# Kernel tuning notes

Measured on AMD Instinct MI355X. Metric: run time of the kernel, lower is better.

## Reference

```python
import jax, jax.numpy as jnp
import numpy as np

B, N, M, C = 4, 4096, 4096, 256
IMG_W, IMG_H = 1242.0, 376.0  # KITTI-like image extents for keypoint coords


def setup_inputs() -> dict:
    key = jax.random.key(0)
    ks = jax.random.split(key, 12)
    s = 1.0 / np.sqrt(C)
    scale_uv = jnp.array([IMG_W, IMG_H], dtype=jnp.float32)
    return {
        "nodes_L": jax.random.normal(ks[0], (B, N, C), jnp.float32),
        "nodes_R": jax.random.normal(ks[1], (B, M, C), jnp.float32),
        "kpts_L": jax.random.uniform(ks[2], (B, N, 2), jnp.float32) * scale_uv,
        "kpts_R": jax.random.uniform(ks[3], (B, M, 2), jnp.float32) * scale_uv,
        "Wq": jax.random.normal(ks[4], (C, C), jnp.float32) * s,
        "bq": jnp.zeros((C,), jnp.float32),
        "Wk": jax.random.normal(ks[5], (C, C), jnp.float32) * s,
        "bk": jnp.zeros((C,), jnp.float32),
        "Wv": jax.random.normal(ks[6], (C, C), jnp.float32) * s,
        "bv": jnp.zeros((C,), jnp.float32),
        "Wm": jax.random.normal(ks[7], (C, C), jnp.float32) * s,
        "bm": jnp.zeros((C,), jnp.float32),
    }


def reference(nodes_L, nodes_R, kpts_L, kpts_R, Wq, bq, Wk, bk, Wv, bv, Wm, bm):
    dim = nodes_L.shape[-1]
    # torch.nn.Linear: y = x @ W.T + b  (W is [out, in])
    Q = jnp.einsum('bnc,dc->bnd', nodes_L, Wq) + bq  # [B,N,C]
    K = jnp.einsum('bmc,dc->bmd', nodes_R, Wk) + bk  # [B,M,C]
    V = jnp.einsum('bmc,dc->bmd', nodes_R, Wv) + bv  # [B,M,C]

    # Epipolar geometric mask from keypoint coordinates
    dist_v = jnp.abs(kpts_L[:, :, 1:2] - kpts_R[:, None, :, 1])  # [B,N,M]
    dist_u = kpts_L[:, :, 0:1] - kpts_R[:, None, :, 0]           # [B,N,M]
    mask = (dist_v < 3.0) & (dist_u > 0) & (dist_u < 192)

    attn = jnp.einsum('bnd,bmd->bnm', Q, K) / (dim ** 0.5)       # [B,N,M]
    attn = jnp.where(mask, attn, jnp.float32(-1e9))
    attn_weights = jax.nn.softmax(attn, axis=-1)                 # [B,N,M]

    matched_features = jnp.einsum('bnm,bmd->bnd', attn_weights, V)
    init_disparity = jnp.sum(attn_weights * dist_u, axis=-1, keepdims=True)  # [B,N,1]
    confidence = jnp.any(mask, axis=-1, keepdims=True).astype(jnp.float32)   # [B,N,1]
    out = jnp.einsum('bnd,cd->bnc', matched_features, Wm) + bm   # [B,N,C]
    return (out, init_disparity, confidence, attn_weights)
```

## Files before the change

### kernel.cpp

```cpp
#include <hip/hip_runtime.h>
#include <stdint.h>

#define CAP 192

typedef __attribute__((ext_vector_type(4))) float f32x4;
typedef __attribute__((ext_vector_type(8))) short bf16x8;

__device__ __forceinline__ float bf2f(ushort u) {
  return __uint_as_float(((unsigned)u) << 16);
}
__device__ __forceinline__ ushort f2bf(float f) {
  unsigned u = __float_as_uint(f);
  return (ushort)((u + 0x7fffu + ((u >> 16) & 1u)) >> 16);
}
__device__ __forceinline__ float wredsum(float v) {
#pragma unroll
  for (int o = 32; o; o >>= 1) v += __shfl_xor(v, o);
  return v;
}

template <bool A_BF16, typename OutT>
__device__ __forceinline__ void gemm_body(const void* __restrict__ Av,
                                          const float* __restrict__ Wf,
                                          const float* __restrict__ bias,
                                          OutT* __restrict__ Y, int blk,
                                          ushort* As, ushort* Bs) {
  int tid = threadIdx.x;
  int lane = tid & 63, wid = tid >> 6;
  int bm = blk >> 1, bn = blk & 1;
  int r0 = bm * 128, c0 = bn * 128;
  int wr = wid >> 1, wc = wid & 1;
  f32x4 acc[4][4] = {};
  for (int k0 = 0; k0 < 256; k0 += 32) {
    __syncthreads();
#pragma unroll
    for (int p = 0; p < 2; ++p) {
      int u = p * 2048 + tid * 8;
      int row = u >> 5, col = u & 31;
      if constexpr (A_BF16) {
        *(bf16x8*)&As[u] =
            *(const bf16x8*)((const ushort*)Av + (size_t)(r0 + row) * 256 + k0 + col);
      } else {
        const float* Af = (const float*)Av;
        float4 lo = *(const float4*)(Af + (size_t)(r0 + row) * 256 + k0 + col);
        float4 hi = *(const float4*)(Af + (size_t)(r0 + row) * 256 + k0 + col + 4);
        ushort4 o0 = { f2bf(lo.x), f2bf(lo.y), f2bf(lo.z), f2bf(lo.w) };
        ushort4 o1 = { f2bf(hi.x), f2bf(hi.y), f2bf(hi.z), f2bf(hi.w) };
        *(ushort4*)&As[u] = o0;
        *(ushort4*)&As[u + 4] = o1;
      }
      {
        float4 lo = *(const float4*)(Wf + (size_t)(c0 + row) * 256 + k0 + col);
        float4 hi = *(const float4*)(Wf + (size_t)(c0 + row) * 256 + k0 + col + 4);
        ushort4 o0 = { f2bf(lo.x), f2bf(lo.y), f2bf(lo.z), f2bf(lo.w) };
        ushort4 o1 = { f2bf(hi.x), f2bf(hi.y), f2bf(hi.z), f2bf(hi.w) };
        *(ushort4*)&Bs[u] = o0;
        *(ushort4*)&Bs[u + 4] = o1;
      }
    }
    __syncthreads();
    bf16x8 af[4], bfr[4];
    int rsel = lane & 15, ksel = (lane >> 4) * 8;
#pragma unroll
    for (int m = 0; m < 4; ++m)
      af[m] = *(bf16x8*)&As[(wr * 64 + m * 16 + rsel) * 32 + ksel];
#pragma unroll
    for (int n = 0; n < 4; ++n)
      bfr[n] = *(bf16x8*)&Bs[(wc * 64 + n * 16 + rsel) * 32 + ksel];
#pragma unroll
    for (int m = 0; m < 4; ++m)
#pragma unroll
      for (int n = 0; n < 4; ++n)
        acc[m][n] = __builtin_amdgcn_mfma_f32_16x16x32_bf16(af[m], bfr[n], acc[m][n], 0, 0, 0);
  }
  int rbase = r0 + wr * 64 + ((lane >> 4) * 4);
  int cbase = c0 + wc * 64 + (lane & 15);
#pragma unroll
  for (int n = 0; n < 4; ++n) {
    float bv = bias[cbase + n * 16];
#pragma unroll
    for (int m = 0; m < 4; ++m) {
#pragma unroll
      for (int j = 0; j < 4; ++j) {
        float v = acc[m][n][j] + bv;
        size_t idx = (size_t)(rbase + m * 16 + j) * 256 + (cbase + n * 16);
        if constexpr (sizeof(OutT) == 2) Y[idx] = (OutT)f2bf(v);
        else Y[idx] = (OutT)v;
      }
    }
  }
}

__global__ __launch_bounds__(256, 2) void gemm3(
    const float* __restrict__ nodesL, const float* __restrict__ nodesR,
    const float* __restrict__ Wq, const float* __restrict__ Wk,
    const float* __restrict__ Wv, const float* __restrict__ bq,
    const float* __restrict__ bk, const float* __restrict__ bv,
    ushort* __restrict__ Qb, ushort* __restrict__ Kb, ushort* __restrict__ Vb) {
  __shared__ __align__(16) ushort As[128 * 32];
  __shared__ __align__(16) ushort Bs[128 * 32];
  int which = blockIdx.x >> 8;
  int blk = blockIdx.x & 255;
  const float* A = (which == 0) ? nodesL : nodesR;
  const float* W = (which == 0) ? Wq : (which == 1) ? Wk : Wv;
  const float* bias = (which == 0) ? bq : (which == 1) ? bk : bv;
  ushort* Y = (which == 0) ? Qb : (which == 1) ? Kb : Vb;
  gemm_body<false, ushort>(A, W, bias, Y, blk, As, Bs);
}

__global__ __launch_bounds__(256, 2) void gemm_out(const ushort* __restrict__ A,
                                                   const float* __restrict__ Wm,
                                                   const float* __restrict__ bias,
                                                   float* __restrict__ Y) {
  __shared__ __align__(16) ushort As[128 * 32];
  __shared__ __align__(16) ushort Bs[128 * 32];
  gemm_body<true, float>(A, Wm, bias, Y, blockIdx.x, As, Bs);
}

__global__ __launch_bounds__(256) void sum_nodes(const float* __restrict__ nodesR,
                                                 const float* __restrict__ kptsR,
                                                 float* __restrict__ S,
                                                 float* __restrict__ sumU) {
  int b = blockIdx.x >> 4, ch = blockIdx.x & 15;
  int t = threadIdx.x;
  int c4 = (t & 63) * 4;
  int r0 = b * 4096 + ch * 256 + (t >> 6);
  float4 acc = {0.f, 0.f, 0.f, 0.f};
  for (int k = 0; k < 64; ++k) {
    float4 v = *(const float4*)(nodesR + (size_t)(r0 + k * 4) * 256 + c4);
    acc.x += v.x; acc.y += v.y; acc.z += v.z; acc.w += v.w;
  }
  __shared__ float4 red[256];
  red[t] = acc;
  float u = kptsR[(size_t)(b * 4096 + ch * 256 + t) * 2];
  u = wredsum(u);
  __shared__ float ured[4];
  if ((t & 63) == 0) ured[t >> 6] = u;
  __syncthreads();
  if (t < 64) {
    float4 x = red[t], y = red[t + 64], z = red[t + 128], w = red[t + 192];
    atomicAdd(&S[b * 256 + c4 + 0], x.x + y.x + z.x + w.x);
    atomicAdd(&S[b * 256 + c4 + 1], x.y + y.y + z.y + w.y);
    atomicAdd(&S[b * 256 + c4 + 2], x.z + y.z + z.z + w.z);
    atomicAdd(&S[b * 256 + c4 + 3], x.w + y.w + z.w + w.w);
  }
  if (t == 0) atomicAdd(&sumU[b], ured[0] + ured[1] + ured[2] + ured[3]);
}

__global__ __launch_bounds__(256) void proj_mean(const float* __restrict__ S,
                                                 const float* __restrict__ sumU,
                                                 const float* __restrict__ Wv,
                                                 const float* __restrict__ bv,
                                                 ushort* __restrict__ meanVb,
                                                 float* __restrict__ meanU) {
  int b = blockIdx.x, c = threadIdx.x;
  const float* s = S + b * 256;
  float acc = 0.f;
  for (int k = 0; k < 256; k += 4) {
    float4 w = *(const float4*)(Wv + (size_t)c * 256 + k);
    acc += s[k] * w.x + s[k + 1] * w.y + s[k + 2] * w.z + s[k + 3] * w.w;
  }
  float mv = acc * (1.f / 4096.f) + bv[c];
  meanVb[b * 256 + c] = f2bf(mv);
  if (c == 0) meanU[b] = sumU[b] * (1.f / 4096.f);
}

__global__ __launch_bounds__(512, 2) void attn_rows(
    const float* __restrict__ kptsL, const float* __restrict__ kptsR,
    const ushort* __restrict__ Qb, const ushort* __restrict__ Kb,
    const ushort* __restrict__ Vb, const float* __restrict__ meanU,
    const ushort* __restrict__ meanVb, float* __restrict__ disp_out,
    float* __restrict__ conf_out, ushort* __restrict__ matched,
    int* __restrict__ rowcnt, int2* __restrict__ rowlist) {
  __shared__ float2 kR[4096];
  __shared__ int bufM[8][CAP];
  __shared__ float bufD[8][CAP];
  __shared__ float bufS[8][CAP];
  int tid = threadIdx.x, lane = tid & 63, wid = tid >> 6;
  int b = blockIdx.x >> 9;
  int n = ((blockIdx.x & 511) << 3) + wid;
  int row = (b << 12) + n;
  int bb = b << 12;
  const float2* kRsrc = (const float2*)kptsR + (size_t)bb;
  for (int i = tid; i < 4096; i += 512) kR[i] = kRsrc[i];
  __syncthreads();
  float2 kL = ((const float2*)kptsL)[(size_t)row];
  ushort4 qv = *(const ushort4*)(Qb + (size_t)row * 256 + lane * 4);
  float q0 = bf2f(qv.x), q1 = bf2f(qv.y), q2 = bf2f(qv.z), q3 = bf2f(qv.w);

  unsigned long long lmask = (1ull << lane) - 1ull;
  int cnt = 0;
#pragma unroll 4
  for (int m0 = 0; m0 < 4096; m0 += 64) {
    float2 kr = kR[m0 + lane];
    float dv = fabsf(kL.y - kr.y);
    float du = kL.x - kr.x;
    bool hit = (dv < 3.0f) && (du > 0.0f) && (du < 192.0f);
    unsigned long long bal = __ballot(hit);
    int pos = cnt + (int)__popcll(bal & lmask);
    if (hit && pos < CAP) { bufM[wid][pos] = m0 + lane; bufD[wid][pos] = du; }
    cnt += (int)__popcll(bal);
  }
  if (cnt > CAP) cnt = CAP;

  float conf, disp;
  if (cnt == 0) {
    conf = 0.f;
    disp = kL.x - meanU[b];
    if (lane == 0) rowcnt[row] = 0;
    ushort4 st = *(const ushort4*)(meanVb + b * 256 + lane * 4);
    *(ushort4*)(matched + (size_t)row * 256 + lane * 4) = st;
  } else {
    float mx = -1e30f;
    int i = 0;
    for (; i + 1 < cnt; i += 2) {
      int ma = bufM[wid][i], mb = bufM[wid][i + 1];
      ushort4 ka = *(const ushort4*)(Kb + ((size_t)(bb + ma)) * 256 + lane * 4);
      ushort4 kb2 = *(const ushort4*)(Kb + ((size_t)(bb + mb)) * 256 + lane * 4);
      float pa = q0 * bf2f(ka.x) + q1 * bf2f(ka.y) + q2 * bf2f(ka.z) + q3 * bf2f(ka.w);
      float pb = q0 * bf2f(kb2.x) + q1 * bf2f(kb2.y) + q2 * bf2f(kb2.z) + q3 * bf2f(kb2.w);
#pragma unroll
      for (int o = 32; o; o >>= 1) {
        pa += __shfl_xor(pa, o);
        pb += __shfl_xor(pb, o);
      }
      float sa = pa * 0.0625f, sb = pb * 0.0625f;
      if (lane == 0) { bufS[wid][i] = sa; bufS[wid][i + 1] = sb; }
      mx = fmaxf(mx, fmaxf(sa, sb));
    }
    if (i < cnt) {
      int ma = bufM[wid][i];
      ushort4 ka = *(const ushort4*)(Kb + ((size_t)(bb + ma)) * 256 + lane * 4);
      float pa = q0 * bf2f(ka.x) + q1 * bf2f(ka.y) + q2 * bf2f(ka.z) + q3 * bf2f(ka.w);
      pa = wredsum(pa);
      float sa = pa * 0.0625f;
      if (lane == 0) bufS[wid][i] = sa;
      mx = fmaxf(mx, sa);
    }
    float psum = 0.f, pdisp = 0.f;
    for (int k = lane; k < cnt; k += 64) {
      float e = expf(bufS[wid][k] - mx);
      bufS[wid][k] = e;
      psum += e;
      pdisp += e * bufD[wid][k];
    }
    psum = wredsum(psum);
    pdisp = wredsum(pdisp);
    float inv = 1.f / psum;
    disp = pdisp * inv;
    conf = 1.f;
    for (int k = lane; k < cnt; k += 64) {
      int2 e;
      e.x = bufM[wid][k];
      e.y = __float_as_int(bufS[wid][k] * inv);
      rowlist[(size_t)row * CAP + k] = e;
    }
    if (lane == 0) rowcnt[row] = cnt;
    float a0 = 0.f, a1 = 0.f, a2 = 0.f, a3 = 0.f;
    i = 0;
    for (; i + 1 < cnt; i += 2) {
      float wa = bufS[wid][i] * inv, wb = bufS[wid][i + 1] * inv;
      int ma = bufM[wid][i], mb = bufM[wid][i + 1];
      ushort4 va = *(const ushort4*)(Vb + ((size_t)(bb + ma)) * 256 + lane * 4);
      ushort4 vb2 = *(const ushort4*)(Vb + ((size_t)(bb + mb)) * 256 + lane * 4);
      a0 += wa * bf2f(va.x) + wb * bf2f(vb2.x);
      a1 += wa * bf2f(va.y) + wb * bf2f(vb2.y);
      a2 += wa * bf2f(va.z) + wb * bf2f(vb2.z);
      a3 += wa * bf2f(va.w) + wb * bf2f(vb2.w);
    }
    if (i < cnt) {
      float wa = bufS[wid][i] * inv;
      int ma = bufM[wid][i];
      ushort4 va = *(const ushort4*)(Vb + ((size_t)(bb + ma)) * 256 + lane * 4);
      a0 += wa * bf2f(va.x); a1 += wa * bf2f(va.y);
      a2 += wa * bf2f(va.z); a3 += wa * bf2f(va.w);
    }
    ushort4 st = { f2bf(a0), f2bf(a1), f2bf(a2), f2bf(a3) };
    *(ushort4*)(matched + (size_t)row * 256 + lane * 4) = st;
  }
  if (lane == 0) { disp_out[row] = disp; conf_out[row] = conf; }
}

__global__ __launch_bounds__(256) void fill_attn(const int* __restrict__ rowcnt,
                                                 float* __restrict__ attn) {
  int r0 = blockIdx.x * 8;
  int tid = threadIdx.x;
#pragma unroll
  for (int r = 0; r < 8; ++r) {
    int row = r0 + r;
    float fill = (rowcnt[row] == 0) ? (1.f / 4096.f) : 0.f;
    f32x4 fv = { fill, fill, fill, fill };
    f32x4* dst = (f32x4*)(attn + (size_t)row * 4096);
#pragma unroll
    for (int j = 0; j < 4; ++j)
      __builtin_nontemporal_store(fv, dst + j * 256 + tid);
  }
}

__global__ __launch_bounds__(256) void scatter_attn(const int* __restrict__ rowcnt,
                                                    const int2* __restrict__ rowlist,
                                                    float* __restrict__ attn) {
  int lane = threadIdx.x & 63;
  for (int row = blockIdx.x * 4 + (threadIdx.x >> 6); row < 16384; row += gridDim.x * 4) {
    int cnt = rowcnt[row];
    for (int i = lane; i < cnt; i += 64) {
      int2 e = rowlist[(size_t)row * CAP + i];
      attn[(size_t)row * 4096 + e.x] = __int_as_float(e.y);
    }
  }
}

extern "C" void kernel_launch(void* const* d_in, const int* in_sizes, int n_in,
                              void* d_out, int out_size, void* d_ws, size_t ws_size,
                              hipStream_t stream) {
  const float* nodes_L = (const float*)d_in[0];
  const float* nodes_R = (const float*)d_in[1];
  const float* kpts_L = (const float*)d_in[2];
  const float* kpts_R = (const float*)d_in[3];
  const float* Wq = (const float*)d_in[4];
  const float* bq = (const float*)d_in[5];
  const float* Wk = (const float*)d_in[6];
  const float* bk = (const float*)d_in[7];
  const float* Wv = (const float*)d_in[8];
  const float* bv = (const float*)d_in[9];
  const float* Wm = (const float*)d_in[10];
  const float* bm = (const float*)d_in[11];

  float* out = (float*)d_out;
  float* disp = out + 4194304;
  float* conf = disp + 16384;
  float* attn = conf + 16384;

  char* ws = (char*)d_ws;
  ushort* Qb = (ushort*)(ws + 0);
  ushort* Kb = (ushort*)(ws + 8388608);
  ushort* Vb = (ushort*)(ws + 16777216);
  ushort* matched = (ushort*)(ws + 25165824);
  float* S = (float*)(ws + 33554432);
  float* sumU = (float*)(ws + 33558528);
  float* meanU = (float*)(ws + 33558592);
  ushort* meanVb = (ushort*)(ws + 33558656);
  int* rowcnt = (int*)(ws + 33562624);
  int2* rowlist = (int2*)(ws + 33628160);

  (void)hipMemsetAsync(S, 0, 4096 + 64, stream);
  sum_nodes<<<64, 256, 0, stream>>>(nodes_R, kpts_R, S, sumU);
  gemm3<<<768, 256, 0, stream>>>(nodes_L, nodes_R, Wq, Wk, Wv, bq, bk, bv, Qb, Kb, Vb);
  proj_mean<<<4, 256, 0, stream>>>(S, sumU, Wv, bv, meanVb, meanU);
  attn_rows<<<2048, 512, 0, stream>>>(kpts_L, kpts_R, Qb, Kb, Vb, meanU, meanVb,
                                      disp, conf, matched, rowcnt, rowlist);
  fill_attn<<<2048, 256, 0, stream>>>(rowcnt, attn);
  scatter_attn<<<512, 256, 0, stream>>>(rowcnt, rowlist, attn);
  gemm_out<<<256, 256, 0, stream>>>(matched, Wm, bm, out);
}
```

Before: 481.8 us.

## Fuse attention-matrix fill and scatter into the attention row kernel

The separate fill_attn and scatter_attn kernels and the rowlist/rowcnt intermediate buffers are removed. Each wave now zero-fills its own attention row with nontemporal stores, then writes either the uniform fill or the sparse softmax weights directly, using an s_waitcnt to order the scatter after the fill. The atomic accumulation in sum_nodes is also replaced by per-chunk partial sums reduced in proj_mean, which drops the memset. This saves two kernel launches and the round-trip of the sparse list through global memory, at the cost of more store traffic inside the attention kernel and a reliance on store ordering within a wave.

```diff
diff --git a/kernel.cpp b/kernel.cpp
--- a/kernel.cpp
+++ b/kernel.cpp
@@ -119,8 +119,8 @@
 
 __global__ __launch_bounds__(256) void sum_nodes(const float* __restrict__ nodesR,
                                                  const float* __restrict__ kptsR,
-                                                 float* __restrict__ S,
-                                                 float* __restrict__ sumU) {
+                                                 float* __restrict__ S16,
+                                                 float* __restrict__ sumU16) {
   int b = blockIdx.x >> 4, ch = blockIdx.x & 15;
   int t = threadIdx.x;
   int c4 = (t & 63) * 4;
@@ -139,22 +139,25 @@
   __syncthreads();
   if (t < 64) {
     float4 x = red[t], y = red[t + 64], z = red[t + 128], w = red[t + 192];
-    atomicAdd(&S[b * 256 + c4 + 0], x.x + y.x + z.x + w.x);
-    atomicAdd(&S[b * 256 + c4 + 1], x.y + y.y + z.y + w.y);
-    atomicAdd(&S[b * 256 + c4 + 2], x.z + y.z + z.z + w.z);
-    atomicAdd(&S[b * 256 + c4 + 3], x.w + y.w + z.w + w.w);
-  }
-  if (t == 0) atomicAdd(&sumU[b], ured[0] + ured[1] + ured[2] + ured[3]);
-}
-
-__global__ __launch_bounds__(256) void proj_mean(const float* __restrict__ S,
-                                                 const float* __restrict__ sumU,
+    float4 s = { x.x + y.x + z.x + w.x, x.y + y.y + z.y + w.y,
+                 x.z + y.z + z.z + w.z, x.w + y.w + z.w + w.w };
+    *(float4*)(S16 + (size_t)(b * 16 + ch) * 256 + t * 4) = s;
+  }
+  if (t == 0) sumU16[b * 16 + ch] = ured[0] + ured[1] + ured[2] + ured[3];
+}
+
+__global__ __launch_bounds__(256) void proj_mean(const float* __restrict__ S16,
+                                                 const float* __restrict__ sumU16,
                                                  const float* __restrict__ Wv,
                                                  const float* __restrict__ bv,
                                                  ushort* __restrict__ meanVb,
                                                  float* __restrict__ meanU) {
   int b = blockIdx.x, c = threadIdx.x;
-  const float* s = S + b * 256;
+  __shared__ float s[256];
+  float a0 = 0.f;
+  for (int ch = 0; ch < 16; ++ch) a0 += S16[(size_t)(b * 16 + ch) * 256 + c];
+  s[c] = a0;
+  __syncthreads();
   float acc = 0.f;
   for (int k = 0; k < 256; k += 4) {
     float4 w = *(const float4*)(Wv + (size_t)c * 256 + k);
@@ -162,16 +165,20 @@
   }
   float mv = acc * (1.f / 4096.f) + bv[c];
   meanVb[b * 256 + c] = f2bf(mv);
-  if (c == 0) meanU[b] = sumU[b] * (1.f / 4096.f);
-}
-
-__global__ __launch_bounds__(512, 2) void attn_rows(
+  if (c == 0) {
+    float su = 0.f;
+    for (int ch = 0; ch < 16; ++ch) su += sumU16[b * 16 + ch];
+    meanU[b] = su * (1.f / 4096.f);
+  }
+}
+
+__global__ __launch_bounds__(512, 2) void attn_fused(
     const float* __restrict__ kptsL, const float* __restrict__ kptsR,
     const ushort* __restrict__ Qb, const ushort* __restrict__ Kb,
     const ushort* __restrict__ Vb, const float* __restrict__ meanU,
     const ushort* __restrict__ meanVb, float* __restrict__ disp_out,
     float* __restrict__ conf_out, ushort* __restrict__ matched,
-    int* __restrict__ rowcnt, int2* __restrict__ rowlist) {
+    float* __restrict__ attn) {
   __shared__ float2 kR[4096];
   __shared__ int bufM[8][CAP];
   __shared__ float bufD[8][CAP];
@@ -181,6 +188,16 @@
   int n = ((blockIdx.x & 511) << 3) + wid;
   int row = (b << 12) + n;
   int bb = b << 12;
+
+  float* rowp = attn + (size_t)row * 4096;
+  {
+    f32x4 zv = {0.f, 0.f, 0.f, 0.f};
+    f32x4* dst = (f32x4*)rowp;
+#pragma unroll
+    for (int j = 0; j < 16; ++j)
+      __builtin_nontemporal_store(zv, dst + j * 64 + lane);
+  }
+
   const float2* kRsrc = (const float2*)kptsR + (size_t)bb;
   for (int i = tid; i < 4096; i += 512) kR[i] = kRsrc[i];
   __syncthreads();
@@ -207,9 +224,15 @@
   if (cnt == 0) {
     conf = 0.f;
     disp = kL.x - meanU[b];
-    if (lane == 0) rowcnt[row] = 0;
     ushort4 st = *(const ushort4*)(meanVb + b * 256 + lane * 4);
     *(ushort4*)(matched + (size_t)row * 256 + lane * 4) = st;
+    asm volatile("s_waitcnt vmcnt(0)" ::: "memory");
+    const float fill = 1.f / 4096.f;
+    f32x4 fv = { fill, fill, fill, fill };
+    f32x4* dst = (f32x4*)rowp;
+#pragma unroll
+    for (int j = 0; j < 16; ++j)
+      __builtin_nontemporal_store(fv, dst + j * 64 + lane);
   } else {
     float mx = -1e30f;
     int i = 0;
@@ -249,17 +272,11 @@
     float inv = 1.f / psum;
     disp = pdisp * inv;
     conf = 1.f;
-    for (int k = lane; k < cnt; k += 64) {
-      int2 e;
-      e.x = bufM[wid][k];
-      e.y = __float_as_int(bufS[wid][k] * inv);
-      rowlist[(size_t)row * CAP + k] = e;
-    }
-    if (lane == 0) rowcnt[row] = cnt;
+    for (int k = lane; k < cnt; k += 64) bufS[wid][k] *= inv;
     float a0 = 0.f, a1 = 0.f, a2 = 0.f, a3 = 0.f;
     i = 0;
     for (; i + 1 < cnt; i += 2) {
-      float wa = bufS[wid][i] * inv, wb = bufS[wid][i + 1] * inv;
+      float wa = bufS[wid][i], wb = bufS[wid][i + 1];
       int ma = bufM[wid][i], mb = bufM[wid][i + 1];
       ushort4 va = *(const ushort4*)(Vb + ((size_t)(bb + ma)) * 256 + lane * 4);
       ushort4 vb2 = *(const ushort4*)(Vb + ((size_t)(bb + mb)) * 256 + lane * 4);
@@ -269,7 +286,7 @@
       a3 += wa * bf2f(va.w) + wb * bf2f(vb2.w);
     }
     if (i < cnt) {
-      float wa = bufS[wid][i] * inv;
+      float wa = bufS[wid][i];
       int ma = bufM[wid][i];
       ushort4 va = *(const ushort4*)(Vb + ((size_t)(bb + ma)) * 256 + lane * 4);
       a0 += wa * bf2f(va.x); a1 += wa * bf2f(va.y);
@@ -277,37 +294,11 @@
     }
     ushort4 st = { f2bf(a0), f2bf(a1), f2bf(a2), f2bf(a3) };
     *(ushort4*)(matched + (size_t)row * 256 + lane * 4) = st;
+    asm volatile("s_waitcnt vmcnt(0)" ::: "memory");
+    for (int k = lane; k < cnt; k += 64)
+      rowp[bufM[wid][k]] = bufS[wid][k];
   }
   if (lane == 0) { disp_out[row] = disp; conf_out[row] = conf; }
-}
-
-__global__ __launch_bounds__(256) void fill_attn(const int* __restrict__ rowcnt,
-                                                 float* __restrict__ attn) {
-  int r0 = blockIdx.x * 8;
-  int tid = threadIdx.x;
-#pragma unroll
-  for (int r = 0; r < 8; ++r) {
-    int row = r0 + r;
-    float fill = (rowcnt[row] == 0) ? (1.f / 4096.f) : 0.f;
-    f32x4 fv = { fill, fill, fill, fill };
-    f32x4* dst = (f32x4*)(attn + (size_t)row * 4096);
-#pragma unroll
-    for (int j = 0; j < 4; ++j)
-      __builtin_nontemporal_store(fv, dst + j * 256 + tid);
-  }
-}
-
-__global__ __launch_bounds__(256) void scatter_attn(const int* __restrict__ rowcnt,
-                                                    const int2* __restrict__ rowlist,
-                                                    float* __restrict__ attn) {
-  int lane = threadIdx.x & 63;
-  for (int row = blockIdx.x * 4 + (threadIdx.x >> 6); row < 16384; row += gridDim.x * 4) {
-    int cnt = rowcnt[row];
-    for (int i = lane; i < cnt; i += 64) {
-      int2 e = rowlist[(size_t)row * CAP + i];
-      attn[(size_t)row * 4096 + e.x] = __int_as_float(e.y);
-    }
-  }
 }
 
 extern "C" void kernel_launch(void* const* d_in, const int* in_sizes, int n_in,
@@ -336,20 +327,15 @@
   ushort* Kb = (ushort*)(ws + 8388608);
   ushort* Vb = (ushort*)(ws + 16777216);
   ushort* matched = (ushort*)(ws + 25165824);
-  float* S = (float*)(ws + 33554432);
-  float* sumU = (float*)(ws + 33558528);
-  float* meanU = (float*)(ws + 33558592);
-  ushort* meanVb = (ushort*)(ws + 33558656);
-  int* rowcnt = (int*)(ws + 33562624);
-  int2* rowlist = (int2*)(ws + 33628160);
-
-  (void)hipMemsetAsync(S, 0, 4096 + 64, stream);
-  sum_nodes<<<64, 256, 0, stream>>>(nodes_R, kpts_R, S, sumU);
+  float* S16 = (float*)(ws + 33554432);
+  float* sumU16 = (float*)(ws + 33620224);
+  float* meanU = (float*)(ws + 33620480);
+  ushort* meanVb = (ushort*)(ws + 33620544);
+
+  sum_nodes<<<64, 256, 0, stream>>>(nodes_R, kpts_R, S16, sumU16);
   gemm3<<<768, 256, 0, stream>>>(nodes_L, nodes_R, Wq, Wk, Wv, bq, bk, bv, Qb, Kb, Vb);
-  proj_mean<<<4, 256, 0, stream>>>(S, sumU, Wv, bv, meanVb, meanU);
-  attn_rows<<<2048, 512, 0, stream>>>(kpts_L, kpts_R, Qb, Kb, Vb, meanU, meanVb,
-                                      disp, conf, matched, rowcnt, rowlist);
-  fill_attn<<<2048, 256, 0, stream>>>(rowcnt, attn);
-  scatter_attn<<<512, 256, 0, stream>>>(rowcnt, rowlist, attn);
+  proj_mean<<<4, 256, 0, stream>>>(S16, sumU16, Wv, bv, meanVb, meanU);
+  attn_fused<<<2048, 512, 0, stream>>>(kpts_L, kpts_R, Qb, Kb, Vb, meanU, meanVb,
+                                       disp, conf, matched, attn);
   gemm_out<<<256, 256, 0, stream>>>(matched, Wm, bm, out);
 }
```

New measurement: 438.2 us. 1.1x faster.
